# Kernel tuning notes

Measured on AMD Instinct MI355X. Metric: run time of the kernel, lower is better.

## Reference

```python
import jax, jax.numpy as jnp
import numpy as np

RBF_GAMMA = 0.001  # initial_gamma_value
DIAG_VALUE = 0.1


def setup_inputs() -> dict:
    key = jax.random.key(0)
    k_x, k_w1, k_b1, k_w2 = jax.random.split(key, 4)
    B, N, T, D = 8, 4096, 128, 32  # batch, nodes, in_dim, latent_dim
    x = jax.random.normal(k_x, (B, N, T), dtype=jnp.float32)
    # nn.Linear params; stored as (in, out) so proj = x @ W + b
    W1 = jax.random.normal(k_w1, (T, D), dtype=jnp.float32) * (2.0 / T) ** 0.5
    W2 = jax.random.normal(k_w2, (T, D), dtype=jnp.float32) * (2.0 / T) ** 0.5
    b1 = jnp.zeros((D,), dtype=jnp.float32)
    b2 = jnp.zeros((D,), dtype=jnp.float32)
    return {"x": x, "W1": W1, "b1": b1, "W2": W2, "b2": b2}


def reference(x, W1, b1, W2, b2):
    # proj1, proj2: (B, N, D)
    p1 = jnp.einsum("bnt,td->bnd", x, W1) + b1
    p2 = jnp.einsum("bnt,td->bnd", x, W2) + b2
    # RBF kernel: exp(-gamma * ||p1_i - p2_j||^2), computed via the
    # algebraic rewrite ||a||^2 + ||b||^2 - 2 a.b (no (B,N,N,D) diff tensor).
    sq1 = jnp.sum(p1 * p1, axis=-1)  # (B, N)
    sq2 = jnp.sum(p2 * p2, axis=-1)  # (B, N)
    dot = jnp.einsum("bnd,bmd->bnm", p1, p2)  # (B, N, N)
    dist_sq = jnp.maximum(sq1[:, :, None] + sq2[:, None, :] - 2.0 * dot, 0.0)
    sim = jnp.exp(-RBF_GAMMA * dist_sq)  # (B, N, N)
    sim = sim.mean(axis=0)  # (N, N)
    # fill_diagonal_(0.1)
    n = sim.shape[0]
    idx = jnp.arange(n)
    sim = sim.at[idx, idx].set(DIAG_VALUE)
    return sim
```

## Files before the change

### kernel.cpp

```cpp
#include <hip/hip_runtime.h>
#include <hip/hip_bf16.h>

typedef __bf16 bf16x8 __attribute__((ext_vector_type(8)));
typedef float  f32x4  __attribute__((ext_vector_type(4)));

constexpr int B = 8, N = 4096, T = 128, D = 32;
constexpr float GAMMA = 0.001f;
constexpr float LOG2E = 1.4426950408889634f;
constexpr float K2 = -GAMMA * LOG2E;
constexpr float M2 = -2.0f * K2;

__device__ __forceinline__ float exp2_fast(float t) {
#if __has_builtin(__builtin_amdgcn_exp2f)
  return __builtin_amdgcn_exp2f(t);
#else
  return exp2f(t);
#endif
}

__device__ __forceinline__ float exp2_poly(float t) {
  return fmaf(fmaf(fmaf(0.0285860f, t, 0.2107500f), t, 0.6821055f), t,
              0.9993455f);
}

__global__ __launch_bounds__(256, 2) void proj_mfma(
    const float* __restrict__ x,  const float* __restrict__ W1,
    const float* __restrict__ b1, const float* __restrict__ W2,
    const float* __restrict__ b2,
    __bf16* __restrict__ p1b, __bf16* __restrict__ p2b,
    float* __restrict__ s1, float* __restrict__ e2) {
  __shared__ bf16x8 wlds[4][4][64];
  const int tid  = threadIdx.x;
  const int lane = tid & 63;
  const int wid  = tid >> 6;
  const int lr   = lane & 15;
  const int lk   = lane >> 4;
  const int r0   = blockIdx.x * 64 + wid * 16;

  #pragma unroll
  for (int t = 0; t < 4; ++t) {
    const int e  = tid + t * 256;
    const int c  = e >> 8;
    const int s  = (e >> 6) & 3;
    const int ln = e & 63;
    const int llr = ln & 15, llk = ln >> 4;
    const float* Wp = (c < 2) ? W1 : W2;
    const int cc = (c * 16 + llr) & 31;
    bf16x8 v;
    #pragma unroll
    for (int j = 0; j < 8; ++j)
      v[j] = (__bf16)Wp[(s * 32 + llk * 8 + j) * D + cc];
    wlds[c][s][ln] = v;
  }
  __syncthreads();

  bf16x8 wf[4][4];
  #pragma unroll
  for (int c = 0; c < 4; ++c)
    #pragma unroll
    for (int s = 0; s < 4; ++s)
      wf[c][s] = wlds[c][s][lane];

  bf16x8 af[4];
  const float* xr = x + (size_t)(r0 + lr) * T;
  #pragma unroll
  for (int s = 0; s < 4; ++s) {
    const int t0 = s * 32 + lk * 8;
    const f32x4 v0 = *reinterpret_cast<const f32x4*>(xr + t0);
    const f32x4 v1 = *reinterpret_cast<const f32x4*>(xr + t0 + 4);
    #pragma unroll
    for (int j = 0; j < 4; ++j) {
      af[s][j]     = (__bf16)v0[j];
      af[s][4 + j] = (__bf16)v1[j];
    }
  }

  f32x4 pv[4];
  #pragma unroll
  for (int c = 0; c < 4; ++c) {
    const float* bp = (c < 2) ? b1 : b2;
    const float bv = bp[(c * 16 + lr) & 31];
    f32x4 accv = {bv, bv, bv, bv};
    #pragma unroll
    for (int s = 0; s < 4; ++s)
      accv = __builtin_amdgcn_mfma_f32_16x16x32_bf16(af[s], wf[c][s], accv, 0, 0, 0);
    pv[c] = accv;
  }

  #pragma unroll
  for (int c = 0; c < 2; ++c)
    #pragma unroll
    for (int r = 0; r < 4; ++r)
      p1b[(size_t)(r0 + lk * 4 + r) * D + c * 16 + lr] = (__bf16)(M2 * pv[c][r]);
  #pragma unroll
  for (int c = 2; c < 4; ++c)
    #pragma unroll
    for (int r = 0; r < 4; ++r)
      p2b[(size_t)(r0 + lk * 4 + r) * D + (c - 2) * 16 + lr] = (__bf16)pv[c][r];

  float q1[4], q2[4];
  #pragma unroll
  for (int r = 0; r < 4; ++r) {
    q1[r] = fmaf(pv[0][r], pv[0][r], pv[1][r] * pv[1][r]);
    q2[r] = fmaf(pv[2][r], pv[2][r], pv[3][r] * pv[3][r]);
  }
  #pragma unroll
  for (int m = 1; m < 16; m <<= 1)
    #pragma unroll
    for (int r = 0; r < 4; ++r) {
      q1[r] += __shfl_xor(q1[r], m, 64);
      q2[r] += __shfl_xor(q2[r], m, 64);
    }
  if (lr == 0) {
    #pragma unroll
    for (int r = 0; r < 4; ++r) {
      const int row = r0 + lk * 4 + r;
      s1[row] = K2 * q1[r];
      e2[row] = 0.125f * exp2_fast(K2 * q2[r]);
    }
  }
}

__global__ __launch_bounds__(256, 3) void fused_kernel(
    const __bf16* __restrict__ p1b, const __bf16* __restrict__ p2b,
    const float* __restrict__ s1,   const float* __restrict__ e2,
    float* __restrict__ out) {
  __shared__ __align__(16) __bf16 LB[B * 64 * 32];
  __shared__ __align__(16) float  LS[B * 128];
  __shared__ __align__(16) float  LE[B * 64];

  const int tid  = threadIdx.x;
  const int lane = tid & 63;
  const int wid  = tid >> 6;
  const int j0 = blockIdx.x * 64;
  const int i0blk = blockIdx.y * 128;
  const int i0 = i0blk + wid * 32;
  const int lr = lane & 15;
  const int lk = lane >> 4;

  #pragma unroll
  for (int q = 0; q < 8; ++q) {
    const int g   = tid + q * 256;
    const int b   = g >> 8;
    const int c8  = g & 255;
    const int row = c8 >> 2;
    const int sl  = c8 & 3;
    const bf16x8 v = *reinterpret_cast<const bf16x8*>(
        p2b + ((size_t)b * N + j0 + row) * D + sl * 8);
    const int su = sl ^ ((row >> 1) & 3);
    *reinterpret_cast<bf16x8*>(&LB[(((b << 6) + row) << 2 | su) << 3]) = v;
  }
  {
    const int b = tid >> 5, o = (tid & 31) * 4;
    *reinterpret_cast<f32x4*>(&LS[b * 128 + o]) =
        *reinterpret_cast<const f32x4*>(s1 + (size_t)b * N + i0blk + o);
  }
  if (tid < 128) {
    const int b = tid >> 4, o = (tid & 15) * 4;
    *reinterpret_cast<f32x4*>(&LE[b * 64 + o]) =
        *reinterpret_cast<const f32x4*>(e2 + (size_t)b * N + j0 + o);
  }
  bf16x8 Areg[B][2];
  #pragma unroll
  for (int b = 0; b < B; ++b)
    #pragma unroll
    for (int a = 0; a < 2; ++a)
      Areg[b][a] = *reinterpret_cast<const bf16x8*>(
          p1b + ((size_t)b * N + i0 + a * 16 + lr) * D + lk * 8);

  __syncthreads();

  f32x4 acc[2][4];
  #pragma unroll
  for (int a = 0; a < 2; ++a)
    #pragma unroll
    for (int c = 0; c < 4; ++c)
      acc[a][c] = f32x4{0.f, 0.f, 0.f, 0.f};

  const int sub = lk ^ ((lr >> 1) & 3);
  #pragma unroll
  for (int b = 0; b < B; ++b) {
    bf16x8 Bf[4];
    #pragma unroll
    for (int c = 0; c < 4; ++c)
      Bf[c] = *reinterpret_cast<const bf16x8*>(
          &LB[(((b << 6) + c * 16 + lr) << 2 | sub) << 3]);
    f32x4 S[2];
    #pragma unroll
    for (int a = 0; a < 2; ++a)
      S[a] = *reinterpret_cast<const f32x4*>(
          &LS[b * 128 + wid * 32 + a * 16 + lk * 4]);
    float E[4];
    #pragma unroll
    for (int c = 0; c < 4; ++c)
      E[c] = LE[b * 64 + c * 16 + lr];

    #pragma unroll
    for (int a = 0; a < 2; ++a) {
      #pragma unroll
      for (int c = 0; c < 4; ++c) {
        f32x4 t = __builtin_amdgcn_mfma_f32_16x16x32_bf16(
            Areg[b][a], Bf[c], S[a], 0, 0, 0);
        #pragma unroll
        for (int r = 0; r < 4; ++r)
          acc[a][c][r] = fmaf(E[c], exp2_poly(t[r]), acc[a][c][r]);
      }
    }
  }

  const bool hasdiag = (i0 < j0 + 64) && (j0 < i0 + 32);
  #pragma unroll
  for (int a = 0; a < 2; ++a) {
    #pragma unroll
    for (int c = 0; c < 4; ++c) {
      #pragma unroll
      for (int r = 0; r < 4; ++r) {
        const int row = i0 + a * 16 + lk * 4 + r;
        const int col = j0 + c * 16 + lr;
        float v = acc[a][c][r];
        if (hasdiag && row == col) v = 0.1f;
        out[(size_t)row * N + col] = v;
      }
    }
  }
}

extern "C" void kernel_launch(void* const* d_in, const int* in_sizes, int n_in,
                              void* d_out, int out_size, void* d_ws, size_t ws_size,
                              hipStream_t stream) {
  (void)in_sizes; (void)n_in; (void)out_size; (void)ws_size;
  const float* x  = (const float*)d_in[0];
  const float* W1 = (const float*)d_in[1];
  const float* b1 = (const float*)d_in[2];
  const float* W2 = (const float*)d_in[3];
  const float* b2 = (const float*)d_in[4];
  float* out = (float*)d_out;

  char* ws = (char*)d_ws;
  const size_t pbytes = (size_t)B * N * D * sizeof(__bf16);
  __bf16* p1b = (__bf16*)ws;
  __bf16* p2b = (__bf16*)(ws + pbytes);
  float*  s1  = (float*)(ws + 2 * pbytes);
  float*  e2  = (float*)(ws + 2 * pbytes + (size_t)B * N * sizeof(float));

  proj_mfma<<<(B * N) / 64, 256, 0, stream>>>(x, W1, b1, W2, b2, p1b, p2b, s1, e2);

  dim3 grid(N / 64, N / 128);
  fused_kernel<<<grid, 256, 0, stream>>>(p1b, p2b, s1, e2, out);
}
```

Baseline: 37.33 us.

## Process two row tiles per block to reuse staged p2 and prefetch A

Each block of the fused kernel now covers 256 rows instead of 128, computing two 128-row tiles in sequence against the same LDS-staged p2/e2 column data. This halves the number of blocks and so halves the redundant global loads and LDS staging of p2b and e2. The second tile's p1 fragments are loaded after the first tile's compute and before its store, so the loads can overlap the output writes. The cost is more registers live for the second A tile and a smaller grid with less parallelism.

```diff
diff --git a/kernel.cpp b/kernel.cpp
--- a/kernel.cpp
+++ b/kernel.cpp
@@ -126,17 +126,24 @@
     const float* __restrict__ s1,   const float* __restrict__ e2,
     float* __restrict__ out) {
   __shared__ __align__(16) __bf16 LB[B * 64 * 32];
-  __shared__ __align__(16) float  LS[B * 128];
+  __shared__ __align__(16) float  LS[B][256];
   __shared__ __align__(16) float  LE[B * 64];
 
   const int tid  = threadIdx.x;
   const int lane = tid & 63;
   const int wid  = tid >> 6;
   const int j0 = blockIdx.x * 64;
-  const int i0blk = blockIdx.y * 128;
-  const int i0 = i0blk + wid * 32;
+  const int i0blk = blockIdx.y * 256;
   const int lr = lane & 15;
   const int lk = lane >> 4;
+
+  bf16x8 A0[B][2];
+  #pragma unroll
+  for (int b = 0; b < B; ++b)
+    #pragma unroll
+    for (int a = 0; a < 2; ++a)
+      A0[b][a] = *reinterpret_cast<const bf16x8*>(
+          p1b + ((size_t)b * N + i0blk + wid * 32 + a * 16 + lr) * D + lk * 8);
 
   #pragma unroll
   for (int q = 0; q < 8; ++q) {
@@ -151,78 +158,100 @@
     *reinterpret_cast<bf16x8*>(&LB[(((b << 6) + row) << 2 | su) << 3]) = v;
   }
   {
-    const int b = tid >> 5, o = (tid & 31) * 4;
-    *reinterpret_cast<f32x4*>(&LS[b * 128 + o]) =
+    const int b = tid >> 5, o = (tid & 31) * 8;
+    *reinterpret_cast<f32x4*>(&LS[b][o]) =
         *reinterpret_cast<const f32x4*>(s1 + (size_t)b * N + i0blk + o);
+    *reinterpret_cast<f32x4*>(&LS[b][o + 4]) =
+        *reinterpret_cast<const f32x4*>(s1 + (size_t)b * N + i0blk + o + 4);
   }
   if (tid < 128) {
     const int b = tid >> 4, o = (tid & 15) * 4;
     *reinterpret_cast<f32x4*>(&LE[b * 64 + o]) =
         *reinterpret_cast<const f32x4*>(e2 + (size_t)b * N + j0 + o);
   }
-  bf16x8 Areg[B][2];
-  #pragma unroll
-  for (int b = 0; b < B; ++b)
-    #pragma unroll
-    for (int a = 0; a < 2; ++a)
-      Areg[b][a] = *reinterpret_cast<const bf16x8*>(
-          p1b + ((size_t)b * N + i0 + a * 16 + lr) * D + lk * 8);
 
   __syncthreads();
 
   f32x4 acc[2][4];
+  const int sub = lk ^ ((lr >> 1) & 3);
+
+  auto compute = [&](const bf16x8 (&A)[B][2], int t)
+      __attribute__((always_inline)) {
+    #pragma unroll
+    for (int b = 0; b < B; ++b) {
+      bf16x8 Bf[4];
+      #pragma unroll
+      for (int c = 0; c < 4; ++c)
+        Bf[c] = *reinterpret_cast<const bf16x8*>(
+            &LB[(((b << 6) + c * 16 + lr) << 2 | sub) << 3]);
+      f32x4 S[2];
+      #pragma unroll
+      for (int a = 0; a < 2; ++a)
+        S[a] = *reinterpret_cast<const f32x4*>(
+            &LS[b][t * 128 + wid * 32 + a * 16 + lk * 4]);
+      float E[4];
+      #pragma unroll
+      for (int c = 0; c < 4; ++c)
+        E[c] = LE[b * 64 + c * 16 + lr];
+
+      #pragma unroll
+      for (int a = 0; a < 2; ++a) {
+        #pragma unroll
+        for (int c = 0; c < 4; ++c) {
+          f32x4 tt = __builtin_amdgcn_mfma_f32_16x16x32_bf16(
+              A[b][a], Bf[c], S[a], 0, 0, 0);
+          #pragma unroll
+          for (int r = 0; r < 4; ++r)
+            acc[a][c][r] = fmaf(E[c], exp2_poly(tt[r]), acc[a][c][r]);
+        }
+      }
+    }
+  };
+
+  auto store_tile = [&](int t) __attribute__((always_inline)) {
+    const int i0 = i0blk + t * 128 + wid * 32;
+    const bool hasdiag = (i0 < j0 + 64) && (j0 < i0 + 32);
+    #pragma unroll
+    for (int a = 0; a < 2; ++a) {
+      #pragma unroll
+      for (int c = 0; c < 4; ++c) {
+        #pragma unroll
+        for (int r = 0; r < 4; ++r) {
+          const int row = i0 + a * 16 + lk * 4 + r;
+          const int col = j0 + c * 16 + lr;
+          float v = acc[a][c][r];
+          if (hasdiag && row == col) v = 0.1f;
+          out[(size_t)row * N + col] = v;
+        }
+      }
+    }
+  };
+
   #pragma unroll
   for (int a = 0; a < 2; ++a)
     #pragma unroll
     for (int c = 0; c < 4; ++c)
       acc[a][c] = f32x4{0.f, 0.f, 0.f, 0.f};
-
-  const int sub = lk ^ ((lr >> 1) & 3);
-  #pragma unroll
-  for (int b = 0; b < B; ++b) {
-    bf16x8 Bf[4];
+  compute(A0, 0);
+
+  bf16x8 A1[B][2];
+  #pragma unroll
+  for (int b = 0; b < B; ++b)
+    #pragma unroll
+    for (int a = 0; a < 2; ++a)
+      A1[b][a] = *reinterpret_cast<const bf16x8*>(
+          p1b + ((size_t)b * N + i0blk + 128 + wid * 32 + a * 16 + lr) * D +
+          lk * 8);
+
+  store_tile(0);
+
+  #pragma unroll
+  for (int a = 0; a < 2; ++a)
     #pragma unroll
     for (int c = 0; c < 4; ++c)
-      Bf[c] = *reinterpret_cast<const bf16x8*>(
-          &LB[(((b << 6) + c * 16 + lr) << 2 | sub) << 3]);
-    f32x4 S[2];
-    #pragma unroll
-    for (int a = 0; a < 2; ++a)
-      S[a] = *reinterpret_cast<const f32x4*>(
-          &LS[b * 128 + wid * 32 + a * 16 + lk * 4]);
-    float E[4];
-    #pragma unroll
-    for (int c = 0; c < 4; ++c)
-      E[c] = LE[b * 64 + c * 16 + lr];
-
-    #pragma unroll
-    for (int a = 0; a < 2; ++a) {
-      #pragma unroll
-      for (int c = 0; c < 4; ++c) {
-        f32x4 t = __builtin_amdgcn_mfma_f32_16x16x32_bf16(
-            Areg[b][a], Bf[c], S[a], 0, 0, 0);
-        #pragma unroll
-        for (int r = 0; r < 4; ++r)
-          acc[a][c][r] = fmaf(E[c], exp2_poly(t[r]), acc[a][c][r]);
-      }
-    }
-  }
-
-  const bool hasdiag = (i0 < j0 + 64) && (j0 < i0 + 32);
-  #pragma unroll
-  for (int a = 0; a < 2; ++a) {
-    #pragma unroll
-    for (int c = 0; c < 4; ++c) {
-      #pragma unroll
-      for (int r = 0; r < 4; ++r) {
-        const int row = i0 + a * 16 + lk * 4 + r;
-        const int col = j0 + c * 16 + lr;
-        float v = acc[a][c][r];
-        if (hasdiag && row == col) v = 0.1f;
-        out[(size_t)row * N + col] = v;
-      }
-    }
-  }
+      acc[a][c] = f32x4{0.f, 0.f, 0.f, 0.f};
+  compute(A1, 1);
+  store_tile(1);
 }
 
 extern "C" void kernel_launch(void* const* d_in, const int* in_sizes, int n_in,
@@ -245,6 +274,6 @@
 
   proj_mfma<<<(B * N) / 64, 256, 0, stream>>>(x, W1, b1, W2, b2, p1b, p2b, s1, e2);
 
-  dim3 grid(N / 64, N / 128);
+  dim3 grid(N / 64, N / 256);
   fused_kernel<<<grid, 256, 0, stream>>>(p1b, p2b, s1, e2, out);
 }
```

After: 38.90 us. 1.04x slower.
